# Kernel tuning notes

Measured on AMD Instinct MI355X. Metric: run time of the kernel, lower is better.

The kernel has to match this reference:

```python
import jax, jax.numpy as jnp
import numpy as np

B, V, F = 16384, 20, 15
H = 256

def setup_inputs() -> dict:
    key = jax.random.key(0)
    ks = jax.random.split(key, 16)
    s = 0.05  # small init scale to keep sigmoids/tanh unsaturated
    return {
        "state": jax.random.normal(ks[0], (B, V, F), jnp.float32),
        "W_ih": jax.random.normal(ks[1], (3 * H, F), jnp.float32) * s,
        "W_hh": jax.random.normal(ks[2], (3 * H, H), jnp.float32) * s,
        "b_ih": jax.random.normal(ks[3], (3 * H,), jnp.float32) * s,
        "b_hh": jax.random.normal(ks[4], (3 * H,), jnp.float32) * s,
        "W1": jax.random.normal(ks[5], (1024, H + F), jnp.float32) * s,
        "b1": jax.random.normal(ks[6], (1024,), jnp.float32) * s,
        "W2": jax.random.normal(ks[7], (1024, 1024), jnp.float32) * s,
        "b2": jax.random.normal(ks[8], (1024,), jnp.float32) * s,
        "W3": jax.random.normal(ks[9], (512, 1024), jnp.float32) * s,
        "b3": jax.random.normal(ks[10], (512,), jnp.float32) * s,
        "W4": jax.random.normal(ks[11], (256, 512), jnp.float32) * s,
        "b4": jax.random.normal(ks[12], (256,), jnp.float32) * s,
        "Wp": jax.random.normal(ks[13], (1, 256), jnp.float32) * s,
        "bp": jax.random.normal(ks[14], (1,), jnp.float32) * s,
    }

def reference(state, W_ih, W_hh, b_ih, b_hh, W1, b1, W2, b2, W3, b3, W4, b4, Wp, bp):
    # state: [B, V, F] -- V vehicles per timestep, F=15 features each.
    # Precompute input-side gate pre-activations for all vehicles: [B, V, 3H]
    xg = jnp.einsum('bvf,gf->bvg', state, W_ih) + b_ih
    h0 = jnp.zeros((state.shape[0], H), state.dtype)

    def gru_step(h, xg_t):  # xg_t: [B, 3H]
        hg = h @ W_hh.T + b_hh  # [B, 3H]
        xr, xz, xn = jnp.split(xg_t, 3, axis=-1)
        hr, hz, hn = jnp.split(hg, 3, axis=-1)
        r = jax.nn.sigmoid(xr + hr)
        z = jax.nn.sigmoid(xz + hz)
        n = jnp.tanh(xn + r * hn)
        return (1.0 - z) * n + z * h, None

    h, _ = jax.lax.scan(gru_step, h0, jnp.swapaxes(xg, 0, 1))  # scan over V
    x = jnp.concatenate([state[:, 0, :], h], axis=-1)  # [B, F+H]
    x = jax.nn.relu(x @ W1.T + b1)
    x = jax.nn.relu(x @ W2.T + b2)
    x = jax.nn.relu(x @ W3.T + b3)
    x = jax.nn.relu(x @ W4.T + b4)
    return jnp.tanh(x @ Wp.T + bp)  # [B, action_dim]
```

## Files before the change

kernel.cpp:

```cpp
#include <hip/hip_runtime.h>


typedef __attribute__((ext_vector_type(8))) __bf16 bf16x8;
typedef __attribute__((ext_vector_type(4))) __bf16 bf16x4;
typedef __attribute__((ext_vector_type(4))) float  floatx4;

#define MFMA16(a, b, c) __builtin_amdgcn_mfma_f32_16x16x32_bf16((a), (b), (c), 0, 0, 0)

#define GL_LDS16(g, l)                                                         \
    __builtin_amdgcn_global_load_lds(                                          \
        (const __attribute__((address_space(1))) void*)(g),                    \
        (__attribute__((address_space(3))) void*)(l), 16, 0, 0)

__device__ __forceinline__ float sigmoid_f(float x) { return 1.f / (1.f + __expf(-x)); }
__device__ __forceinline__ float tanh_f(float x)    { return 1.f - 2.f / (1.f + __expf(2.f * x)); }

#define S0 147456u
#define S1 442368u
#define S2 1490944u
#define S3 2015232u
#define S4 2146304u
#define S5 2154496u
#define S6 2220032u
#define S7 2220544u
#define S8 2221056u

__global__ void prep_kernel(const float* __restrict__ W_ih, const float* __restrict__ W_hh,
                            const float* __restrict__ b_ih, const float* __restrict__ b_hh,
                            const float* __restrict__ W1, const float* __restrict__ W2,
                            const float* __restrict__ W3, const float* __restrict__ W4,
                            __bf16* __restrict__ Wg1, __bf16* __restrict__ W1p,
                            __bf16* __restrict__ W2b, __bf16* __restrict__ W3b,
                            __bf16* __restrict__ W4b, __bf16* __restrict__ Win_n,
                            __bf16* __restrict__ Whh_n, float* __restrict__ bsum,
                            float* __restrict__ bihn, float* __restrict__ bhhn)
{
    for (unsigned i = blockIdx.x * blockDim.x + threadIdx.x; i < S8; i += gridDim.x * blockDim.x) {
        if (i < S0) {
            unsigned g = i / 288u, c = i % 288u;
            float v;
            if (c < 15u)       v = W_ih[g * 15u + c];
            else if (c == 15u) v = b_ih[g] + b_hh[g];
            else if (c < 32u)  v = 0.f;
            else               v = W_hh[g * 256u + (c - 32u)];
            Wg1[i] = (__bf16)v;
        } else if (i < S1) {
            unsigned t = i - S0, o = t / 288u, c = t % 288u;
            float v = (c < 15u) ? W1[o * 271u + c] : ((c < 32u) ? 0.f : W1[o * 271u + (c - 17u)]);
            W1p[t] = (__bf16)v;
        } else if (i < S2) {
            unsigned t = i - S1; W2b[t] = (__bf16)W2[t];
        } else if (i < S3) {
            unsigned t = i - S2; W3b[t] = (__bf16)W3[t];
        } else if (i < S4) {
            unsigned t = i - S3; W4b[t] = (__bf16)W4[t];
        } else if (i < S5) {
            unsigned t = i - S4, j = t / 32u, c = t % 32u;
            float v;
            if (c < 15u)       v = W_ih[(512u + j) * 15u + c];
            else if (c == 15u) v = b_ih[512u + j];
            else               v = 0.f;
            Win_n[t] = (__bf16)v;
        } else if (i < S6) {
            unsigned t = i - S5; Whh_n[t] = (__bf16)W_hh[512u * 256u + t];
        } else if (i < S7) {
            unsigned t = i - S6; bsum[t] = b_ih[t] + b_hh[t];
        } else {
            unsigned t = i - S7;
            if (t < 256u) bihn[t] = b_ih[512u + t];
            else          bhhn[t - 256u] = b_hh[512u + t - 256u];
        }
    }
}

#define HSTRIDE 264
#define HBUF_N  (64 * HSTRIDE)
#define SSTRIDE 40
#define SBUF_N  (64 * SSTRIDE)

__global__ __launch_bounds__(1024)
void gru_kernel(const float* __restrict__ state,
                const __bf16* __restrict__ Wg1,  const __bf16* __restrict__ Win_n,
                const __bf16* __restrict__ Whh_n,
                const float* __restrict__ bhhn, __bf16* __restrict__ x0)
{
    __shared__ __bf16 hbuf[2 * HBUF_N];
    __shared__ __bf16 sbuf[2 * SBUF_N];
    __shared__ __bf16 rzbuf[4 * 1024 * 8];

    const int tid  = threadIdx.x;
    const int wave = tid >> 6;
    const int lane = tid & 63;
    const int q    = lane >> 4;
    const int ln   = lane & 15;
    const int b0   = blockIdx.x * 64;

    {
        bf16x8 z = {};
        bf16x8* p = (bf16x8*)hbuf;
        #pragma unroll 3
        for (int i = tid; i < HBUF_N / 8; i += 1024) p[i] = z;
        if (tid < 2 * SBUF_N / 8) ((bf16x8*)sbuf)[tid] = z;
    }
    const int srow = tid >> 4, sk = tid & 15;

    const floatx4 Bhn = *(const floatx4*)(bhhn + wave * 16 + q * 4);

    const int jr = wave * 16 + ln;
    const __bf16* wr = Wg1   + (size_t)jr * 288 + q * 8;
    const __bf16* wz = Wg1   + (size_t)(256 + jr) * 288 + q * 8;
    const __bf16* wx = Win_n + (size_t)jr * 32  + q * 8;
    const __bf16* wh = Whh_n + (size_t)jr * 256 + q * 8;

    const __bf16* hread  = hbuf + ln * HSTRIDE + q * 8;
    __bf16*       hwrite = hbuf + ln * HSTRIDE + wave * 16 + q * 4;
    const __bf16* sread  = sbuf + ln * SSTRIDE + q * 8;
    __bf16*       rzw    = rzbuf + tid * 8;

    if (sk < 15)
        sbuf[srow * SSTRIDE + sk] = (__bf16)state[(size_t)(b0 + srow) * 300 + sk];
    if (tid < 128) sbuf[(tid >> 6) * SBUF_N + (tid & 63) * SSTRIDE + 15] = (__bf16)1.0f;
    __syncthreads();

#define GRU_STEP(v, SB)                                                          \
    {                                                                            \
        float snext = 0.f;                                                       \
        if ((v) < 19 && sk < 15)                                                 \
            snext = state[(size_t)(b0 + srow) * 300 + ((v) + 1) * 15 + sk];      \
        _Pragma("unroll 1")                                                      \
        for (int p = 0; p < 2; ++p) {                                            \
            floatx4 acc0[4], acc1[4];                                            \
            const floatx4 zf = {0.f, 0.f, 0.f, 0.f};                             \
            _Pragma("unroll")                                                    \
            for (int nt = 0; nt < 4; nt++) { acc0[nt] = zf; acc1[nt] = zf; }     \
            if (p == 0) {                                                        \
                {                                                                \
                    bf16x8 a0 = *(const bf16x8*)(wr);                            \
                    bf16x8 a1 = *(const bf16x8*)(wz);                            \
                    _Pragma("unroll")                                            \
                    for (int nt = 0; nt < 4; nt++) {                             \
                        bf16x8 b = *(const bf16x8*)(sread + (SB) * SBUF_N +      \
                                                    nt * (16 * SSTRIDE));        \
                        acc0[nt] = MFMA16(a0, b, acc0[nt]);                      \
                        acc1[nt] = MFMA16(a1, b, acc1[nt]);                      \
                    }                                                            \
                }                                                                \
                _Pragma("unroll")                                                \
                for (int kk = 0; kk < 8; ++kk) {                                 \
                    bf16x8 a0 = *(const bf16x8*)(wr + 32 + kk * 32);             \
                    bf16x8 a1 = *(const bf16x8*)(wz + 32 + kk * 32);             \
                    _Pragma("unroll")                                            \
                    for (int nt = 0; nt < 4; nt++) {                             \
                        bf16x8 b = *(const bf16x8*)(hread + (SB) * HBUF_N +      \
                                                    nt * (16 * HSTRIDE) +        \
                                                    kk * 32);                    \
                        acc0[nt] = MFMA16(a0, b, acc0[nt]);                      \
                        acc1[nt] = MFMA16(a1, b, acc1[nt]);                      \
                    }                                                            \
                }                                                                \
                _Pragma("unroll")                                                \
                for (int nt = 0; nt < 4; nt++) {                                 \
                    bf16x8 rz;                                                   \
                    _Pragma("unroll")                                            \
                    for (int r = 0; r < 4; r++) {                                \
                        rz[r]     = (__bf16)sigmoid_f(acc0[nt][r]);              \
                        rz[4 + r] = (__bf16)sigmoid_f(acc1[nt][r]);              \
                    }                                                            \
                    *(bf16x8*)(rzw + nt * 8192) = rz;                            \
                }                                                                \
            } else {                                                             \
                {                                                                \
                    bf16x8 a0 = *(const bf16x8*)(wx);                            \
                    _Pragma("unroll")                                            \
                    for (int nt = 0; nt < 4; nt++) {                             \
                        bf16x8 b = *(const bf16x8*)(sread + (SB) * SBUF_N +      \
                                                    nt * (16 * SSTRIDE));        \
                        acc0[nt] = MFMA16(a0, b, acc0[nt]);                      \
                    }                                                            \
                }                                                                \
                _Pragma("unroll")                                                \
                for (int kk = 0; kk < 8; ++kk) {                                 \
                    bf16x8 a1 = *(const bf16x8*)(wh + kk * 32);                  \
                    _Pragma("unroll")                                            \
                    for (int nt = 0; nt < 4; nt++) {                             \
                        bf16x8 b = *(const bf16x8*)(hread + (SB) * HBUF_N +      \
                                                    nt * (16 * HSTRIDE) +        \
                                                    kk * 32);                    \
                        acc1[nt] = MFMA16(a1, b, acc1[nt]);                      \
                    }                                                            \
                }                                                                \
                _Pragma("unroll")                                                \
                for (int nt = 0; nt < 4; nt++) {                                 \
                    bf16x8 rz = *(const bf16x8*)(rzw + nt * 8192);               \
                    bf16x4 ho = *(const bf16x4*)(hwrite + (SB) * HBUF_N +        \
                                                 nt * (16 * HSTRIDE));           \
                    bf16x4 hv;                                                   \
                    _Pragma("unroll")                                            \
                    for (int r = 0; r < 4; r++) {                                \
                        float rg = (float)rz[r];                                 \
                        float zg = (float)rz[4 + r];                             \
                        float nn = tanh_f(acc0[nt][r] +                          \
                                          rg * (acc1[nt][r] + Bhn[r]));          \
                        float hnew = (1.f - zg) * nn + zg * (float)ho[r];        \
                        hv[r] = (__bf16)hnew;                                    \
                    }                                                            \
                    *(bf16x4*)(hwrite + (1 - (SB)) * HBUF_N +                    \
                               nt * (16 * HSTRIDE)) = hv;                        \
                }                                                                \
            }                                                                    \
        }                                                                        \
        if ((v) < 19 && sk < 15)                                                 \
            sbuf[(1 - (SB)) * SBUF_N + srow * SSTRIDE + sk] = (__bf16)snext;     \
        __syncthreads();                                                         \
    }

    #pragma unroll 1
    for (int v2 = 0; v2 < 10; ++v2) {
        GRU_STEP(2 * v2,     0)
        GRU_STEP(2 * v2 + 1, 1)
    }
#undef GRU_STEP

    {
        const int erow = tid >> 4, p = tid & 15;
        #pragma unroll
        for (int s = 0; s < 2; s++) {
            const int col = p * 8 + s * 128;
            *(bf16x8*)(x0 + (size_t)(b0 + erow) * 288 + 32 + col) =
                *(const bf16x8*)(hbuf + erow * HSTRIDE + col);
        }
    }
    #pragma unroll
    for (int t = 0; t < 2; t++) {
        int i = tid + t * 1024;
        int erow = i >> 5, c = i & 31;
        float s = (c < 15) ? state[(size_t)(b0 + erow) * 300 + c] : 0.f;
        x0[(size_t)(b0 + erow) * 288 + c] = (__bf16)s;
    }
}

__global__ __launch_bounds__(256)
void gemm_bias_act(const __bf16* __restrict__ A, const __bf16* __restrict__ W,
                   const float* __restrict__ bias, __bf16* __restrict__ C,
                   int N, int K, int relu)
{
    __shared__ __bf16 smem[128 * 136];

    const int tid  = threadIdx.x;
    const int wave = tid >> 6, lane = tid & 63;
    const int q = lane >> 4, ln = lane & 15;
    const int wm = wave >> 1, wn = wave & 1;
    const int arow0 = blockIdx.x * 128;
    const int bcol0 = blockIdx.y * 128;

    float bv[4];
    #pragma unroll
    for (int n = 0; n < 4; n++) bv[n] = bias[bcol0 + wn * 64 + n * 16 + ln];

    floatx4 acc[4][4];
    const floatx4 zf = {0.f, 0.f, 0.f, 0.f};
    #pragma unroll
    for (int m = 0; m < 4; m++)
        #pragma unroll
        for (int n = 0; n < 4; n++) acc[m][n] = zf;

    const int stg_row = wave * 16 + (lane >> 2);
    const int stg_k   = (lane & 3) * 8;
    const int lds_off = wave * 512;

    int kt = 0;
    for (; kt + 64 <= K; kt += 64) {
        #pragma unroll
        for (int h = 0; h < 2; h++)
            #pragma unroll
            for (int rd = 0; rd < 2; rd++) {
                GL_LDS16(A + (size_t)(arow0 + stg_row + rd * 64) * K + kt + h * 32 + stg_k,
                         smem + h * 4096 + lds_off + rd * 2048);
                GL_LDS16(W + (size_t)(bcol0 + stg_row + rd * 64) * K + kt + h * 32 + stg_k,
                         smem + 8192 + h * 4096 + lds_off + rd * 2048);
            }
        __syncthreads();
        #pragma unroll
        for (int h = 0; h < 2; h++) {
            bf16x8 af[4], bf[4];
            #pragma unroll
            for (int m = 0; m < 4; m++)
                af[m] = *(const bf16x8*)(smem + h * 4096 + (wm * 64 + m * 16 + ln) * 32 + q * 8);
            #pragma unroll
            for (int n = 0; n < 4; n++)
                bf[n] = *(const bf16x8*)(smem + 8192 + h * 4096 + (wn * 64 + n * 16 + ln) * 32 + q * 8);
            #pragma unroll
            for (int n = 0; n < 4; n++)
                #pragma unroll
                for (int m = 0; m < 4; m++)
                    acc[m][n] = MFMA16(af[m], bf[n], acc[m][n]);
        }
        __syncthreads();
    }
    if (kt < K) {
        #pragma unroll
        for (int rd = 0; rd < 2; rd++) {
            GL_LDS16(A + (size_t)(arow0 + stg_row + rd * 64) * K + kt + stg_k,
                     smem + lds_off + rd * 2048);
            GL_LDS16(W + (size_t)(bcol0 + stg_row + rd * 64) * K + kt + stg_k,
                     smem + 8192 + lds_off + rd * 2048);
        }
        __syncthreads();
        bf16x8 af[4], bf[4];
        #pragma unroll
        for (int m = 0; m < 4; m++)
            af[m] = *(const bf16x8*)(smem + (wm * 64 + m * 16 + ln) * 32 + q * 8);
        #pragma unroll
        for (int n = 0; n < 4; n++)
            bf[n] = *(const bf16x8*)(smem + 8192 + (wn * 64 + n * 16 + ln) * 32 + q * 8);
        #pragma unroll
        for (int n = 0; n < 4; n++)
            #pragma unroll
            for (int m = 0; m < 4; m++)
                acc[m][n] = MFMA16(af[m], bf[n], acc[m][n]);
        __syncthreads();
    }

    #pragma unroll
    for (int m = 0; m < 4; m++)
        #pragma unroll
        for (int n = 0; n < 4; n++)
            #pragma unroll
            for (int r = 0; r < 4; r++) {
                float val = acc[m][n][r] + bv[n];
                if (relu) val = fmaxf(val, 0.f);
                smem[(wm * 64 + m * 16 + q * 4 + r) * 136 + wn * 64 + n * 16 + ln] = (__bf16)val;
            }
    __syncthreads();
    {
        const int row = tid >> 4, seg = tid & 15;
        #pragma unroll
        for (int p = 0; p < 8; p++) {
            const int rr = row + p * 16;
            *(bf16x8*)(C + (size_t)(arow0 + rr) * N + bcol0 + seg * 8) =
                *(const bf16x8*)(smem + rr * 136 + seg * 8);
        }
    }
}

__global__ __launch_bounds__(256)
void head_kernel(const __bf16* __restrict__ x4, const float* __restrict__ Wp,
                 const float* __restrict__ bp, float* __restrict__ out)
{
    const int tid = threadIdx.x;
    const int wave = tid >> 6, lane = tid & 63;
    const int row = blockIdx.x * 64 + wave * 16 + (lane >> 2);
    const int part = lane & 3;
    const __bf16* xp = x4 + (size_t)row * 256 + part * 64;
    const float* wp = Wp + part * 64;
    float sum = 0.f;
    #pragma unroll
    for (int i = 0; i < 8; i++) {
        bf16x8 xv = *(const bf16x8*)(xp + i * 8);
        #pragma unroll
        for (int jj = 0; jj < 8; jj++) sum += (float)xv[jj] * wp[i * 8 + jj];
    }
    sum += __shfl_xor(sum, 1);
    sum += __shfl_xor(sum, 2);
    if (part == 0) out[row] = tanhf(sum + bp[0]);
}

extern "C" void kernel_launch(void* const* d_in, const int* in_sizes, int n_in,
                              void* d_out, int out_size, void* d_ws, size_t ws_size,
                              hipStream_t stream)
{
    const float* state = (const float*)d_in[0];
    const float* W_ih  = (const float*)d_in[1];
    const float* W_hh  = (const float*)d_in[2];
    const float* b_ih  = (const float*)d_in[3];
    const float* b_hh  = (const float*)d_in[4];
    const float* W1    = (const float*)d_in[5];
    const float* b1    = (const float*)d_in[6];
    const float* W2    = (const float*)d_in[7];
    const float* b2    = (const float*)d_in[8];
    const float* W3    = (const float*)d_in[9];
    const float* b3    = (const float*)d_in[10];
    const float* W4    = (const float*)d_in[11];
    const float* b4    = (const float*)d_in[12];
    const float* Wp    = (const float*)d_in[13];
    const float* bp    = (const float*)d_in[14];
    float* out = (float*)d_out;

    char* ws = (char*)d_ws;
    size_t off = 0;
    auto alloc = [&](size_t bytes) -> void* {
        void* p = ws + off;
        off += (bytes + 255) & ~(size_t)255;
        return p;
    };
    __bf16* Wg1   = (__bf16*)alloc(512 * 288 * 2);
    __bf16* W1p   = (__bf16*)alloc(1024 * 288 * 2);
    __bf16* W2b   = (__bf16*)alloc(1024 * 1024 * 2);
    __bf16* W3b   = (__bf16*)alloc(512 * 1024 * 2);
    __bf16* W4b   = (__bf16*)alloc(256 * 512 * 2);
    __bf16* Win_n = (__bf16*)alloc(256 * 32 * 2);
    __bf16* Whh_n = (__bf16*)alloc(256 * 256 * 2);
    float*  bsum  = (float*)alloc(512 * 4);
    float*  bihn  = (float*)alloc(256 * 4);
    float*  bhhn  = (float*)alloc(256 * 4);
    __bf16* x0    = (__bf16*)alloc((size_t)16384 * 288 * 2);
    __bf16* xA    = (__bf16*)alloc((size_t)16384 * 1024 * 2);
    __bf16* xB    = (__bf16*)alloc((size_t)16384 * 1024 * 2);

    prep_kernel<<<2048, 256, 0, stream>>>(W_ih, W_hh, b_ih, b_hh, W1, W2, W3, W4,
                                          Wg1, W1p, W2b, W3b, W4b, Win_n, Whh_n,
                                          bsum, bihn, bhhn);
    gru_kernel<<<256, 1024, 0, stream>>>(state, Wg1, Win_n, Whh_n, bhhn, x0);
    gemm_bias_act<<<dim3(128, 8), 256, 0, stream>>>(x0, W1p, b1, xA, 1024, 288, 1);
    gemm_bias_act<<<dim3(128, 8), 256, 0, stream>>>(xA, W2b, b2, xB, 1024, 1024, 1);
    gemm_bias_act<<<dim3(128, 4), 256, 0, stream>>>(xB, W3b, b3, xA, 512, 1024, 1);
    gemm_bias_act<<<dim3(128, 2), 256, 0, stream>>>(xA, W4b, b4, xB, 256, 512, 1);
    head_kernel<<<256, 256, 0, stream>>>(xB, Wp, bp, out);
}
```

Measured before the change: 462.4 us.

## Fuse GRU gate passes into one loop and keep gates and h in registers

The GRU step used to run two sequential passes: the first computed r/z and spilled them to a large LDS buffer, the second computed the n-gate contributions and reread r/z and the previous h from LDS. Now one pass over k shares each h B-fragment load across three accumulators (r, z, hn), and the gates are applied directly from registers. The previous h is held in registers (hprev) rather than reread from LDS. This removes the rz LDS traffic and duplicate h-tile reads, and frees LDS that may allow more occupancy. In exchange it needs more accumulator registers (12 floatx4 live plus 4 for ax), which raises register pressure.

```diff
diff --git a/kernel.cpp b/kernel.cpp
--- a/kernel.cpp
+++ b/kernel.cpp
@@ -86,7 +86,6 @@
 {
     __shared__ __bf16 hbuf[2 * HBUF_N];
     __shared__ __bf16 sbuf[2 * SBUF_N];
-    __shared__ __bf16 rzbuf[4 * 1024 * 8];
 
     const int tid  = threadIdx.x;
     const int wave = tid >> 6;
@@ -115,7 +114,10 @@
     const __bf16* hread  = hbuf + ln * HSTRIDE + q * 8;
     __bf16*       hwrite = hbuf + ln * HSTRIDE + wave * 16 + q * 4;
     const __bf16* sread  = sbuf + ln * SSTRIDE + q * 8;
-    __bf16*       rzw    = rzbuf + tid * 8;
+
+    bf16x4 hprev[4];
+    #pragma unroll
+    for (int nt = 0; nt < 4; nt++) hprev[nt] = (bf16x4){};
 
     if (sk < 15)
         sbuf[srow * SSTRIDE + sk] = (__bf16)state[(size_t)(b0 + srow) * 300 + sk];
@@ -127,87 +129,50 @@
         float snext = 0.f;                                                       \
         if ((v) < 19 && sk < 15)                                                 \
             snext = state[(size_t)(b0 + srow) * 300 + ((v) + 1) * 15 + sk];      \
-        _Pragma("unroll 1")                                                      \
-        for (int p = 0; p < 2; ++p) {                                            \
-            floatx4 acc0[4], acc1[4];                                            \
-            const floatx4 zf = {0.f, 0.f, 0.f, 0.f};                             \
+        floatx4 ar[4], az[4], ah[4];                                             \
+        const floatx4 zf = {0.f, 0.f, 0.f, 0.f};                                 \
+        _Pragma("unroll")                                                        \
+        for (int nt = 0; nt < 4; nt++) { ar[nt] = zf; az[nt] = zf; ah[nt] = zf; }\
+        _Pragma("unroll")                                                        \
+        for (int kk = 0; kk < 8; ++kk) {                                         \
+            bf16x8 a0 = *(const bf16x8*)(wr + 32 + kk * 32);                     \
+            bf16x8 a1 = *(const bf16x8*)(wz + 32 + kk * 32);                     \
+            bf16x8 a2 = *(const bf16x8*)(wh + kk * 32);                          \
             _Pragma("unroll")                                                    \
-            for (int nt = 0; nt < 4; nt++) { acc0[nt] = zf; acc1[nt] = zf; }     \
-            if (p == 0) {                                                        \
-                {                                                                \
-                    bf16x8 a0 = *(const bf16x8*)(wr);                            \
-                    bf16x8 a1 = *(const bf16x8*)(wz);                            \
-                    _Pragma("unroll")                                            \
-                    for (int nt = 0; nt < 4; nt++) {                             \
-                        bf16x8 b = *(const bf16x8*)(sread + (SB) * SBUF_N +      \
-                                                    nt * (16 * SSTRIDE));        \
-                        acc0[nt] = MFMA16(a0, b, acc0[nt]);                      \
-                        acc1[nt] = MFMA16(a1, b, acc1[nt]);                      \
-                    }                                                            \
-                }                                                                \
-                _Pragma("unroll")                                                \
-                for (int kk = 0; kk < 8; ++kk) {                                 \
-                    bf16x8 a0 = *(const bf16x8*)(wr + 32 + kk * 32);             \
-                    bf16x8 a1 = *(const bf16x8*)(wz + 32 + kk * 32);             \
-                    _Pragma("unroll")                                            \
-                    for (int nt = 0; nt < 4; nt++) {                             \
-                        bf16x8 b = *(const bf16x8*)(hread + (SB) * HBUF_N +      \
-                                                    nt * (16 * HSTRIDE) +        \
-                                                    kk * 32);                    \
-                        acc0[nt] = MFMA16(a0, b, acc0[nt]);                      \
-                        acc1[nt] = MFMA16(a1, b, acc1[nt]);                      \
-                    }                                                            \
-                }                                                                \
-                _Pragma("unroll")                                                \
-                for (int nt = 0; nt < 4; nt++) {                                 \
-                    bf16x8 rz;                                                   \
-                    _Pragma("unroll")                                            \
-                    for (int r = 0; r < 4; r++) {                                \
-                        rz[r]     = (__bf16)sigmoid_f(acc0[nt][r]);              \
-                        rz[4 + r] = (__bf16)sigmoid_f(acc1[nt][r]);              \
-                    }                                                            \
-                    *(bf16x8*)(rzw + nt * 8192) = rz;                            \
-                }                                                                \
-            } else {                                                             \
-                {                                                                \
-                    bf16x8 a0 = *(const bf16x8*)(wx);                            \
-                    _Pragma("unroll")                                            \
-                    for (int nt = 0; nt < 4; nt++) {                             \
-                        bf16x8 b = *(const bf16x8*)(sread + (SB) * SBUF_N +      \
-                                                    nt * (16 * SSTRIDE));        \
-                        acc0[nt] = MFMA16(a0, b, acc0[nt]);                      \
-                    }                                                            \
-                }                                                                \
-                _Pragma("unroll")                                                \
-                for (int kk = 0; kk < 8; ++kk) {                                 \
-                    bf16x8 a1 = *(const bf16x8*)(wh + kk * 32);                  \
-                    _Pragma("unroll")                                            \
-                    for (int nt = 0; nt < 4; nt++) {                             \
-                        bf16x8 b = *(const bf16x8*)(hread + (SB) * HBUF_N +      \
-                                                    nt * (16 * HSTRIDE) +        \
-                                                    kk * 32);                    \
-                        acc1[nt] = MFMA16(a1, b, acc1[nt]);                      \
-                    }                                                            \
-                }                                                                \
-                _Pragma("unroll")                                                \
-                for (int nt = 0; nt < 4; nt++) {                                 \
-                    bf16x8 rz = *(const bf16x8*)(rzw + nt * 8192);               \
-                    bf16x4 ho = *(const bf16x4*)(hwrite + (SB) * HBUF_N +        \
-                                                 nt * (16 * HSTRIDE));           \
-                    bf16x4 hv;                                                   \
-                    _Pragma("unroll")                                            \
-                    for (int r = 0; r < 4; r++) {                                \
-                        float rg = (float)rz[r];                                 \
-                        float zg = (float)rz[4 + r];                             \
-                        float nn = tanh_f(acc0[nt][r] +                          \
-                                          rg * (acc1[nt][r] + Bhn[r]));          \
-                        float hnew = (1.f - zg) * nn + zg * (float)ho[r];        \
-                        hv[r] = (__bf16)hnew;                                    \
-                    }                                                            \
-                    *(bf16x4*)(hwrite + (1 - (SB)) * HBUF_N +                    \
-                               nt * (16 * HSTRIDE)) = hv;                        \
-                }                                                                \
+            for (int nt = 0; nt < 4; nt++) {                                     \
+                bf16x8 b = *(const bf16x8*)(hread + (SB) * HBUF_N +              \
+                                            nt * (16 * HSTRIDE) + kk * 32);      \
+                ar[nt] = MFMA16(a0, b, ar[nt]);                                  \
+                az[nt] = MFMA16(a1, b, az[nt]);                                  \
+                ah[nt] = MFMA16(a2, b, ah[nt]);                                  \
             }                                                                    \
+        }                                                                        \
+        floatx4 ax[4];                                                           \
+        {                                                                        \
+            bf16x8 a0 = *(const bf16x8*)(wr);                                    \
+            bf16x8 a1 = *(const bf16x8*)(wz);                                    \
+            bf16x8 a2 = *(const bf16x8*)(wx);                                    \
+            _Pragma("unroll")                                                    \
+            for (int nt = 0; nt < 4; nt++) {                                     \
+                bf16x8 b = *(const bf16x8*)(sread + (SB) * SBUF_N +              \
+                                            nt * (16 * SSTRIDE));                \
+                ar[nt] = MFMA16(a0, b, ar[nt]);                                  \
+                az[nt] = MFMA16(a1, b, az[nt]);                                  \
+                ax[nt] = MFMA16(a2, b, zf);                                      \
+            }                                                                    \
+        }                                                                        \
+        _Pragma("unroll")                                                        \
+        for (int nt = 0; nt < 4; nt++) {                                         \
+            bf16x4 hv;                                                           \
+            _Pragma("unroll")                                                    \
+            for (int r = 0; r < 4; r++) {                                        \
+                float rg = sigmoid_f(ar[nt][r]);                                 \
+                float zg = sigmoid_f(az[nt][r]);                                 \
+                float nn = tanh_f(ax[nt][r] + rg * (ah[nt][r] + Bhn[r]));        \
+                hv[r] = (__bf16)((1.f - zg) * nn + zg * (float)hprev[nt][r]);    \
+            }                                                                    \
+            hprev[nt] = hv;                                                      \
+            *(bf16x4*)(hwrite + (1 - (SB)) * HBUF_N + nt * (16 * HSTRIDE)) = hv; \
         }                                                                        \
         if ((v) < 19 && sk < 15)                                                 \
             sbuf[(1 - (SB)) * SBUF_N + srow * SSTRIDE + sk] = (__bf16)snext;     \
```

Measured after the change: 547.7 us. 1.18x slower.
